# Performance work log

Hardware: AMD Instinct MI355X
Metric: run time of the kernel (lower is better)

The kernel has to match this reference:

```python
import jax, jax.numpy as jnp
import numpy as np
from jax import lax

D = 512      # d_model
DSRC = 128   # grapheme vocab
DTGT = 128   # phoneme vocab
B = 1024
TS = 64      # T_src
TT = 64      # T_tgt


def setup_inputs() -> dict:
    key = jax.random.key(0)
    ks = iter(jax.random.split(key, 64))
    def w(shape, s=0.02):
        return (jax.random.normal(next(ks), shape) * s).astype(jnp.float32)
    z = lambda n: jnp.zeros((n,), jnp.float32)
    inp = dict(
        src=jax.random.randint(next(ks), (B, TS), 0, DSRC),
        tgt=jax.random.randint(next(ks), (B, TT), 0, DTGT),
        enc_emb_w=w((DSRC, D)),
        # PyTorch LSTM gate order i,f,g,o; weights stored [in, 4H] for x @ W
        enc_wi_f=w((D, 4 * D)), enc_wh_f=w((D, 4 * D)), enc_bi_f=z(4 * D), enc_bh_f=z(4 * D),
        enc_wi_b=w((D, 4 * D)), enc_wh_b=w((D, 4 * D)), enc_bi_b=z(4 * D), enc_bh_b=z(4 * D),
        enc_post_w=w((2 * D, D)), enc_post_b=z(D),
        h_post_w=w((2 * D, D)), h_post_b=z(D),
        c_post_w=w((2 * D, D)), c_post_b=z(D),
        wq_w=w((D, D)), wq_b=z(D),
        wk_w=w((D, D)), wk_b=z(D),
        wv_w=w((D, D)), wv_b=z(D),
        wo_w=w((D, D)), wo_b=z(D),
        dec_emb_w=w((DTGT, D)),
        dec_wi=w((2 * D, 4 * D)), dec_wh=w((D, 4 * D)), dec_bi=z(4 * D), dec_bh=z(4 * D),
        dec_post_w=w((D, DTGT)), dec_post_b=z(DTGT),
    )
    return inp


def _lstm_cell(x, h, c, Wi, Wh, b):
    g = x @ Wi + h @ Wh + b
    i, f, gg, o = jnp.split(g, 4, axis=-1)
    c = jax.nn.sigmoid(f) * c + jax.nn.sigmoid(i) * jnp.tanh(gg)
    h = jax.nn.sigmoid(o) * jnp.tanh(c)
    return h, c


def _lstm_scan(x, h0, c0, Wi, Wh, b):
    # x: [B,T,Din] -> ys: [B,T,H], final (h,c)
    def step(carry, xt):
        h, c = _lstm_cell(xt, carry[0], carry[1], Wi, Wh, b)
        return (h, c), h
    (h, c), ys = lax.scan(step, (h0, c0), jnp.swapaxes(x, 0, 1))
    return jnp.swapaxes(ys, 0, 1), h, c


def reference(src, tgt, enc_emb_w,
              enc_wi_f, enc_wh_f, enc_bi_f, enc_bh_f,
              enc_wi_b, enc_wh_b, enc_bi_b, enc_bh_b,
              enc_post_w, enc_post_b, h_post_w, h_post_b, c_post_w, c_post_b,
              wq_w, wq_b, wk_w, wk_b, wv_w, wv_b, wo_w, wo_b,
              dec_emb_w, dec_wi, dec_wh, dec_bi, dec_bh, dec_post_w, dec_post_b):
    b, d = src.shape[0], enc_emb_w.shape[1]
    scale = d ** -0.5
    z0 = jnp.zeros((b, d), enc_emb_w.dtype)

    # --- bi-LSTM encoder (dropout = identity in eval) ---
    emb = enc_emb_w[src]                                   # [B,TS,D]
    fwd, hf, cf = _lstm_scan(emb, z0, z0, enc_wi_f, enc_wh_f, enc_bi_f + enc_bh_f)
    bwd, hb, cb = _lstm_scan(emb[:, ::-1], z0, z0, enc_wi_b, enc_wh_b, enc_bi_b + enc_bh_b)
    bwd = bwd[:, ::-1]
    enc_out = jnp.concatenate([fwd, bwd], -1) @ enc_post_w + enc_post_b   # [B,TS,D]
    h = jnp.tanh(jnp.concatenate([hf, hb], -1) @ h_post_w + h_post_b)     # [B,D]
    c = jnp.tanh(jnp.concatenate([cf, cb], -1) @ c_post_w + c_post_b)

    # attention K/V projections of enc_out are step-invariant: compute once
    K = enc_out @ wk_w + wk_b
    V = enc_out @ wv_w + wv_b
    dec_b = dec_bi + dec_bh

    prev = dec_emb_w[tgt[:, 0]]                            # [B,D]

    def dec_step(carry, _):
        prev, h, c = carry
        q = prev @ wq_w + wq_b                             # [B,D]
        score = jax.nn.softmax(jnp.einsum('bd,btd->bt', q, K) * scale)  # [B,TS]
        ctx = jnp.einsum('bt,btd->bd', score, V) @ wo_w + wo_b
        x = jnp.concatenate([prev, ctx], -1)               # [B,2D]
        h, c = _lstm_cell(x, h, c, dec_wi, dec_wh, dec_b)
        out = h @ dec_post_w + dec_post_b                  # [B,DTGT]
        prev = dec_emb_w[jnp.argmax(out, -1)]
        return (prev, h, c), (score, out)

    _, (attn_res, res) = lax.scan(dec_step, (prev, h, c), None, length=tgt.shape[1])
    attn_res = jnp.swapaxes(attn_res, 0, 1)                # [B,TT,TS]
    res = jnp.swapaxes(res, 0, 1)                          # [B,TT,DTGT]
    return attn_res, res
```

## Files before the change

kernel.cpp:

```cpp
#include <hip/hip_runtime.h>
#include <hip/hip_bf16.h>

namespace k77 {

typedef long long ll;
typedef double f64x4 __attribute__((ext_vector_type(4)));

constexpr int D    = 512;
constexpr int DTGT = 128;
constexpr int NB   = 1024;
constexpr int TS   = 64;
constexpr int TT   = 64;
constexpr int G4   = 2048;

__global__ void probe_mfma(int* __restrict__ dlay)
{
    __shared__ double ref[256];
    __shared__ int ok[4];
    const int l = threadIdx.x;
    const int l15 = l & 15, l4 = l >> 4;
    if (l < 4) ok[l] = 1;
    double a = 1.0 + 3.0 * l15 + 7.0 * l4;
    double b = 2.0 + 5.0 * l15 + 11.0 * l4;
    f64x4 d = {0.0, 0.0, 0.0, 0.0};
    d = __builtin_amdgcn_mfma_f64_16x16x4f64(a, b, d, 0, 0, 0);
    if (l < 16) {
        for (int j = 0; j < 16; ++j) {
            double s = 0.0;
            for (int k = 0; k < 4; ++k)
                s += (1.0 + 3.0 * l + 7.0 * k) * (2.0 + 5.0 * j + 11.0 * k);
            ref[l * 16 + j] = s;
        }
    }
    __syncthreads();
#pragma unroll
    for (int n = 0; n < 4; ++n) {
        if (d[n] != ref[(l4 * 4 + n) * 16 + l15]) atomicAnd(&ok[0], 0);
        if (d[n] != ref[(l4 + 4 * n) * 16 + l15]) atomicAnd(&ok[1], 0);
        if (d[n] != ref[l15 * 16 + (l4 * 4 + n)]) atomicAnd(&ok[2], 0);
        if (d[n] != ref[l15 * 16 + (l4 + 4 * n)]) atomicAnd(&ok[3], 0);
    }
    __syncthreads();
    if (l == 0) {
        int r = -1;
        for (int i = 3; i >= 0; --i) if (ok[i]) r = i;
        *dlay = r;
    }
}

__global__ void dlay_check(const int* __restrict__ dlay, float* __restrict__ out0)
{
    if (*dlay < 0)
        for (int i = threadIdx.x; i < 256; i += 64) out0[i] = 3.0e38f;
}

__device__ __forceinline__ void dmap(int dl, int l15, int l4, int n, int& r, int& c)
{
    if (dl == 1)      { r = l4 + 4 * n;  c = l15; }
    else if (dl == 2) { r = l15;         c = l4 * 4 + n; }
    else if (dl == 3) { r = l15;         c = l4 + 4 * n; }
    else              { r = l4 * 4 + n;  c = l15; }
}

__global__ void tab_gemm64(const float* __restrict__ A, const float* __restrict__ B,
                           const float* __restrict__ b1, const float* __restrict__ b2,
                           float* __restrict__ C, int M, int N, int K, int ldc, float scale, int perm)
{
    int j = blockIdx.x * 256 + threadIdx.x;
    int m = blockIdx.y;
    if (j >= N || m >= M) return;
    const float* ar = A + (size_t)m * K;
    double acc = 0.0;
    for (int k = 0; k < K; ++k) acc += (double)ar[k] * (double)B[(size_t)k * N + j];
    if (b1) acc += (double)b1[j];
    if (b2) acc += (double)b2[j];
    int j2 = perm ? ((j & 511) * 4 + (j >> 9)) : j;
    C[(size_t)m * ldc + j2] = (float)(acc * (double)scale);
}

struct Tab3 { const float *A0,*A1,*A2,*B0,*B1,*B2,*p0,*p1,*p2,*q0,*q1,*q2; float *C0,*C1,*C2; };
__global__ void tab3_gemm64(Tab3 t)
{
    int j = blockIdx.x * 256 + threadIdx.x;
    int m = blockIdx.y;
    int z = blockIdx.z;
    const float* A  = z == 0 ? t.A0 : (z == 1 ? t.A1 : t.A2);
    const float* B  = z == 0 ? t.B0 : (z == 1 ? t.B1 : t.B2);
    const float* b1 = z == 0 ? t.p0 : (z == 1 ? t.p1 : t.p2);
    const float* b2 = z == 0 ? t.q0 : (z == 1 ? t.q1 : t.q2);
    float*       C  = z == 0 ? t.C0 : (z == 1 ? t.C1 : t.C2);
    const float* ar = A + (size_t)m * D;
    double acc = 0.0;
    for (int k = 0; k < D; ++k) acc += (double)ar[k] * (double)B[(size_t)k * G4 + j];
    acc += (double)b1[j];
    acc += (double)b2[j];
    C[(size_t)m * G4 + (j & 511) * 4 + (j >> 9)] = (float)acc;
}

struct Perm4 { const float *i0,*i1,*i2,*i3; float *o0,*o1,*o2,*o3; int r0,r1,r2,r3; };
__global__ void permW4(Perm4 p)
{
    int j = blockIdx.x * 256 + threadIdx.x;
    int k = blockIdx.y;
    int z = blockIdx.z;
    const float* in = z == 0 ? p.i0 : (z == 1 ? p.i1 : (z == 2 ? p.i2 : p.i3));
    float*      out = z == 0 ? p.o0 : (z == 1 ? p.o1 : (z == 2 ? p.o2 : p.o3));
    int      rowoff = z == 0 ? p.r0 : (z == 1 ? p.r1 : (z == 2 ? p.r2 : p.r3));
    out[(size_t)k * G4 + (j & 511) * 4 + (j >> 9)] = in[(size_t)(k + rowoff) * G4 + j];
}

__global__ void init_kv(const float* __restrict__ bkvo, __hip_bfloat16* __restrict__ Kb,
                        float* __restrict__ Vb)
{
    for (ll i = (ll)blockIdx.x * 256 + threadIdx.x; i < (ll)NB * TS * D; i += (ll)gridDim.x * 256) {
        int d = (int)(i & (D - 1));
        Kb[i] = __float2bfloat16(bkvo[d]);
        Vb[i] = bkvo[D + d];
    }
}

template<int USE2>
__device__ __forceinline__ void gates_body(
    double* smem, const float* a0, const float* a1,
    const float* B0, const float* B1,
    const float* tab, const int* idx, int idxStride,
    float* cb, float* hb, int bx, int by, int K, int useC, int dl, int tid)
{
    float* As = (float*)smem;
    float* Bs = As + 64 * 34;
    const int row0 = by * 64, col0 = bx * 32;
    const int wave = tid >> 6, lane = tid & 63;
    const int wr = wave >> 1, wc = wave & 1;
    const int l15 = lane & 15, l4 = lane >> 4;

    f64x4 acc[2];
    acc[0] = (f64x4){0.0, 0.0, 0.0, 0.0};
    acc[1] = (f64x4){0.0, 0.0, 0.0, 0.0};

    for (int k0 = 0; k0 < K; k0 += 32) {
#pragma unroll
        for (int l = 0; l < 8; ++l) {
            int t = tid + l * 256;
            int k = t & 31, m = t >> 5;
            int kk = k0 + k;
            float v;
            if (USE2 && kk >= D) v = a1[(size_t)(row0 + m) * D + (kk - D)];
            else                 v = a0[(size_t)(row0 + m) * D + kk];
            As[m * 34 + k] = v;
        }
#pragma unroll
        for (int l = 0; l < 4; ++l) {
            int t = tid + l * 256;
            int j = t & 31, kr = t >> 5;
            int kk = k0 + kr;
            float v;
            if (USE2 && kk >= D) v = B1[(size_t)(kk - D) * G4 + col0 + j];
            else                 v = B0[(size_t)kk * G4 + col0 + j];
            Bs[j * 35 + kr] = v;
        }
        __syncthreads();
#pragma unroll
        for (int kk4 = 0; kk4 < 8; ++kk4) {
            const int kr = kk4 * 4 + l4;
            double a0f = (double)As[(wr * 32 + l15) * 34 + kr];
            double a1f = (double)As[(wr * 32 + 16 + l15) * 34 + kr];
            double b0f = (double)Bs[(wc * 16 + l15) * 35 + kr];
            acc[0] = __builtin_amdgcn_mfma_f64_16x16x4f64(a0f, b0f, acc[0], 0, 0, 0);
            acc[1] = __builtin_amdgcn_mfma_f64_16x16x4f64(a1f, b0f, acc[1], 0, 0, 0);
        }
        __syncthreads();
    }

    float* G = (float*)smem;
#pragma unroll
    for (int tr = 0; tr < 2; ++tr)
#pragma unroll
        for (int n = 0; n < 4; ++n) {
            int r, c;
            dmap(dl, l15, l4, n, r, c);
            int lr = wr * 32 + tr * 16 + r;
            int lc = wc * 16 + c;
            const float* trw = tab + (size_t)idx[(size_t)(row0 + lr) * idxStride] * G4;
            G[lr * 33 + lc] = (float)(acc[tr][n] + (double)trw[col0 + lc]);
        }
    __syncthreads();

    const int ty = tid >> 3, tx = tid & 7;
    const int d  = (col0 + tx * 4) >> 2;
#pragma unroll
    for (int i = 0; i < 2; ++i) {
        int rl  = ty * 2 + i;
        int row = row0 + rl;
        float gi = G[rl * 33 + tx * 4 + 0];
        float gf = G[rl * 33 + tx * 4 + 1];
        float gg = G[rl * 33 + tx * 4 + 2];
        float go = G[rl * 33 + tx * 4 + 3];
        float c  = useC ? cb[(size_t)row * D + d] : 0.f;
        float si = 1.f / (1.f + expf(-gi));
        float sf = 1.f / (1.f + expf(-gf));
        float so = 1.f / (1.f + expf(-go));
        c = sf * c + si * tanhf(gg);
        cb[(size_t)row * D + d] = c;
        hb[(size_t)row * D + d] = so * tanhf(c);
    }
}

__device__ __forceinline__ void fold_body(
    double* smem, const float* h, const float* W, int rowoff,
    __hip_bfloat16* Kb, float* Vb, int trow, int bx, int by, int dl, int tid)
{
    float* As = (float*)smem;
    float* Bs = As + 64 * 34;
    const int row0 = by * 64, col0 = bx * 64;
    const int wave = tid >> 6, lane = tid & 63;
    const int wr = wave >> 1, wc = wave & 1;
    const int l15 = lane & 15, l4 = lane >> 4;

    f64x4 acc[2][2];
#pragma unroll
    for (int i = 0; i < 2; ++i)
#pragma unroll
        for (int j = 0; j < 2; ++j) acc[i][j] = (f64x4){0.0, 0.0, 0.0, 0.0};

    for (int k0 = 0; k0 < D; k0 += 32) {
#pragma unroll
        for (int l = 0; l < 8; ++l) {
            int t = tid + l * 256;
            {   int k = t & 31, m = t >> 5;
                As[m * 34 + k] = h[(size_t)(row0 + m) * D + k0 + k];
            }
            {   int j = t & 63, kr = t >> 6;
                Bs[j * 35 + kr] = W[(size_t)(rowoff + k0 + kr) * 1024 + col0 + j];
            }
        }
        __syncthreads();
#pragma unroll
        for (int kk4 = 0; kk4 < 8; ++kk4) {
            const int kr = kk4 * 4 + l4;
            double a0f = (double)As[(wr * 32 + l15) * 34 + kr];
            double a1f = (double)As[(wr * 32 + 16 + l15) * 34 + kr];
            double b0f = (double)Bs[(wc * 32 + l15) * 35 + kr];
            double b1f = (double)Bs[(wc * 32 + 16 + l15) * 35 + kr];
            acc[0][0] = __builtin_amdgcn_mfma_f64_16x16x4f64(a0f, b0f, acc[0][0], 0, 0, 0);
            acc[0][1] = __builtin_amdgcn_mfma_f64_16x16x4f64(a0f, b1f, acc[0][1], 0, 0, 0);
            acc[1][0] = __builtin_amdgcn_mfma_f64_16x16x4f64(a1f, b0f, acc[1][0], 0, 0, 0);
            acc[1][1] = __builtin_amdgcn_mfma_f64_16x16x4f64(a1f, b1f, acc[1][1], 0, 0, 0);
        }
        __syncthreads();
    }

#pragma unroll
    for (int tr = 0; tr < 2; ++tr)
#pragma unroll
        for (int tc = 0; tc < 2; ++tc)
#pragma unroll
            for (int n = 0; n < 4; ++n) {
                int r, c;
                dmap(dl, l15, l4, n, r, c);
                int row = row0 + wr * 32 + tr * 16 + r;
                int col = col0 + wc * 32 + tc * 16 + c;
                double v = acc[tr][tc][n];
                ll ix = ((ll)row * TS + trow) * D + (col & (D - 1));
                if (col < D) {
                    double v2 = v + (double)__bfloat162float(Kb[ix]);
                    Kb[ix] = __float2bfloat16((float)v2);
                } else {
                    Vb[ix] = (float)((double)Vb[ix] + v);
                }
            }
}

struct EncArgs {
    const float *hFr, *hBr;
    float *hFw, *hBw, *cF, *cB;
    const float *WhPf, *WhPb, *tabPf, *tabPb;
    const int *srcF, *srcB;
    const float *WKVo;
    __hip_bfloat16 *Kb; float *Vb;
    int foldF, foldB;
    int K, useC, nG;
    const int *dlayp;
};

__global__ __launch_bounds__(256)
void enc_mega(EncArgs a)
{
    __shared__ double smem[2208];
    const int bid = blockIdx.x;
    const int tid = threadIdx.x;
    const int dl  = a.dlayp[0];
    if (bid < a.nG) {
        const int dir = bid >> 10;
        const int tt  = bid & 1023;
        gates_body<0>(smem,
                      dir ? a.hBr : a.hFr, nullptr,
                      dir ? a.WhPb : a.WhPf, nullptr,
                      dir ? a.tabPb : a.tabPf,
                      dir ? a.srcB : a.srcF, TS,
                      dir ? a.cB : a.cF,
                      dir ? a.hBw : a.hFw,
                      tt & 63, tt >> 6, a.K, a.useC, dl, tid);
    } else {
        const int ff = bid - a.nG;
        const int fz = ff >> 8;
        fold_body(smem, fz ? a.hBr : a.hFr, a.WKVo, fz ? D : 0,
                  a.Kb, a.Vb, fz ? a.foldB : a.foldF,
                  ff & 15, (ff >> 4) & 15, dl, tid);
    }
}

struct DGArgs {
    const float *ctx, *h;
    const float *wiP, *whP, *tabP;
    const int *amax;
    float *cdec, *hw;
    const int *dlayp;
};

__global__ __launch_bounds__(256)
void dec_gates(DGArgs a)
{
    __shared__ double smem[1648];
    const int bid = blockIdx.x;
    gates_body<1>(smem, a.ctx, a.h, a.wiP, a.whP, a.tabP,
                  a.amax, 1, a.cdec, a.hw, bid & 63, bid >> 6, 2 * D, 1,
                  a.dlayp[0], threadIdx.x);
}

__global__ void attn_kernel(const float* __restrict__ qtab, const int* __restrict__ amax,
                            const __hip_bfloat16* __restrict__ Kb, const float* __restrict__ Vb,
                            float* __restrict__ aout, int step, float* __restrict__ ctx)
{
    const int b = blockIdx.x, tid = threadIdx.x;
    __shared__ float qs[D];
    __shared__ float ss[TS];
    qs[tid] = qtab[(size_t)amax[b] * D + tid];
    __syncthreads();
    const int t = tid >> 3, l8 = tid & 7;
    const __hip_bfloat16* krow = Kb + ((size_t)b * TS + t) * D;
    double acc = 0.0;
    for (int d = l8; d < D; d += 8) acc += (double)qs[d] * (double)__bfloat162float(krow[d]);
    acc += __shfl_xor(acc, 4);
    acc += __shfl_xor(acc, 2);
    acc += __shfl_xor(acc, 1);
    if (l8 == 0) ss[t] = (float)acc;
    __syncthreads();
    if (tid < TS) {
        float v = ss[tid], mx = v;
#pragma unroll
        for (int o = 32; o; o >>= 1) mx = fmaxf(mx, __shfl_xor(mx, o));
        float e = expf(v - mx), sm = e;
#pragma unroll
        for (int o = 32; o; o >>= 1) sm += __shfl_xor(sm, o);
        float sc = e / sm;
        ss[tid] = sc;
        aout[((size_t)b * TT + step) * TS + tid] = sc;
    }
    __syncthreads();
    double a = 0.0;
    const float* vcol = Vb + (size_t)b * TS * D + tid;
    for (int t2 = 0; t2 < TS; ++t2) a += (double)ss[t2] * (double)vcol[(size_t)t2 * D];
    ctx[(size_t)b * D + tid] = (float)a;
}

__global__ __launch_bounds__(512)
void out_attn(const float* __restrict__ h, const float* __restrict__ W,
              const float* __restrict__ bias, float* __restrict__ res,
              int step, int* __restrict__ amax,
              const float* __restrict__ qtab, const __hip_bfloat16* __restrict__ Kb,
              const float* __restrict__ Vb, float* __restrict__ aout,
              float* __restrict__ ctx, int doAttn)
{
    const int b = blockIdx.x, tid = threadIdx.x;
    __shared__ float hs[D];
    __shared__ double vals[DTGT];
    __shared__ int tok;
    __shared__ float qs[D];
    __shared__ float ss[TS];

    hs[tid] = h[(size_t)b * D + tid];
    __syncthreads();
    if (tid < DTGT) {
        double acc = (double)bias[tid];
        for (int k = 0; k < D; ++k) acc += (double)hs[k] * (double)W[(size_t)k * DTGT + tid];
        vals[tid] = acc;
        res[((size_t)b * TT + step) * DTGT + tid] = (float)acc;
    }
    __syncthreads();
    if (tid == 0) {
        double best = vals[0]; int bi = 0;
        for (int j = 1; j < DTGT; ++j) if (vals[j] > best) { best = vals[j]; bi = j; }
        amax[b] = bi;
        tok = bi;
    }
    __syncthreads();

    if (!doAttn) return;

    qs[tid] = qtab[(size_t)tok * D + tid];
    __syncthreads();
    const int t = tid >> 3, l8 = tid & 7;
    const __hip_bfloat16* krow = Kb + ((size_t)b * TS + t) * D;
    double acc = 0.0;
    for (int d = l8; d < D; d += 8) acc += (double)qs[d] * (double)__bfloat162float(krow[d]);
    acc += __shfl_xor(acc, 4);
    acc += __shfl_xor(acc, 2);
    acc += __shfl_xor(acc, 1);
    if (l8 == 0) ss[t] = (float)acc;
    __syncthreads();
    if (tid < TS) {
        float v = ss[tid], mx = v;
#pragma unroll
        for (int o = 32; o; o >>= 1) mx = fmaxf(mx, __shfl_xor(mx, o));
        float e = expf(v - mx), sm = e;
#pragma unroll
        for (int o = 32; o; o >>= 1) sm += __shfl_xor(sm, o);
        float sc = e / sm;
        ss[tid] = sc;
        aout[((size_t)b * TT + (step + 1)) * TS + tid] = sc;
    }
    __syncthreads();
    double a = 0.0;
    const float* vcol = Vb + (size_t)b * TS * D + tid;
    for (int t2 = 0; t2 < TS; ++t2) a += (double)ss[t2] * (double)vcol[(size_t)t2 * D];
    ctx[(size_t)b * D + tid] = (float)a;
}

__global__ __launch_bounds__(512)
void hc_init(const float* __restrict__ hF, const float* __restrict__ hB,
             const float* __restrict__ cF, const float* __restrict__ cB,
             const float* __restrict__ hpw, const float* __restrict__ hpb,
             const float* __restrict__ cpw, const float* __restrict__ cpb,
             float* __restrict__ h0, float* __restrict__ c0)
{
    __shared__ float s0[D], s1[D], s2[D], s3[D];
    const int b = blockIdx.x, j = threadIdx.x;
    s0[j] = hF[(size_t)b * D + j]; s1[j] = hB[(size_t)b * D + j];
    s2[j] = cF[(size_t)b * D + j]; s3[j] = cB[(size_t)b * D + j];
    __syncthreads();
    double a = (double)hpb[j];
    for (int k = 0; k < D; ++k) a += (double)s0[k] * (double)hpw[(size_t)k * D + j];
    for (int k = 0; k < D; ++k) a += (double)s1[k] * (double)hpw[(size_t)(k + D) * D + j];
    h0[(size_t)b * D + j] = (float)tanh(a);
    a = (double)cpb[j];
    for (int k = 0; k < D; ++k) a += (double)s2[k] * (double)cpw[(size_t)k * D + j];
    for (int k = 0; k < D; ++k) a += (double)s3[k] * (double)cpw[(size_t)(k + D) * D + j];
    c0[(size_t)b * D + j] = (float)tanh(a);
}

__global__ void init_amax(const int* __restrict__ tgt, int* __restrict__ amax)
{
    int b = blockIdx.x * 256 + threadIdx.x;
    if (b < NB) amax[b] = tgt[(size_t)b * TT];
}

}

extern "C" void kernel_launch(void* const* d_in, const int* in_sizes, int n_in,
                              void* d_out, int out_size, void* d_ws, size_t ws_size,
                              hipStream_t stream)
{
    using namespace k77;
    (void)in_sizes; (void)n_in; (void)out_size;

    const int*   src        = (const int*)  d_in[0];
    const int*   tgt        = (const int*)  d_in[1];
    const float* enc_emb_w  = (const float*)d_in[2];
    const float* enc_wi_f   = (const float*)d_in[3];
    const float* enc_wh_f   = (const float*)d_in[4];
    const float* enc_bi_f   = (const float*)d_in[5];
    const float* enc_bh_f   = (const float*)d_in[6];
    const float* enc_wi_b   = (const float*)d_in[7];
    const float* enc_wh_b   = (const float*)d_in[8];
    const float* enc_bi_b   = (const float*)d_in[9];
    const float* enc_bh_b   = (const float*)d_in[10];
    const float* enc_post_w = (const float*)d_in[11];
    const float* enc_post_b = (const float*)d_in[12];
    const float* h_post_w   = (const float*)d_in[13];
    const float* h_post_b   = (const float*)d_in[14];
    const float* c_post_w   = (const float*)d_in[15];
    const float* c_post_b   = (const float*)d_in[16];
    const float* wq_w       = (const float*)d_in[17];
    const float* wq_b       = (const float*)d_in[18];
    const float* wk_w       = (const float*)d_in[19];
    const float* wk_b       = (const float*)d_in[20];
    const float* wv_w       = (const float*)d_in[21];
    const float* wv_b       = (const float*)d_in[22];
    const float* wo_w       = (const float*)d_in[23];
    const float* wo_b       = (const float*)d_in[24];
    const float* dec_emb_w  = (const float*)d_in[25];
    const float* dec_wi     = (const float*)d_in[26];
    const float* dec_wh     = (const float*)d_in[27];
    const float* dec_bi     = (const float*)d_in[28];
    const float* dec_bh     = (const float*)d_in[29];
    const float* dec_post_w = (const float*)d_in[30];
    const float* dec_post_b = (const float*)d_in[31];

    float* ws = (float*)d_ws;
    size_t off = 0;
    auto alloc = [&](size_t n) { float* p = ws + off; off += n; return p; };
    float* hF0     = alloc((size_t)NB * D);
    float* hF1     = alloc((size_t)NB * D);
    float* hB0     = alloc((size_t)NB * D);
    float* hB1     = alloc((size_t)NB * D);
    float* cF      = alloc((size_t)NB * D);
    float* cB      = alloc((size_t)NB * D);
    float* hd0     = alloc((size_t)NB * D);
    float* hd1     = alloc((size_t)NB * D);
    float* cdec    = alloc((size_t)NB * D);
    float* ctxb    = alloc((size_t)NB * D);
    float* tabPf   = alloc((size_t)128 * G4);
    float* tabPb   = alloc((size_t)128 * G4);
    float* dec_tabP= alloc((size_t)128 * G4);
    float* q_tab   = alloc((size_t)128 * D);
    float* WKVo    = alloc((size_t)1024 * 1024);
    float* bkvo    = alloc(1024);
    float* WhPf    = alloc((size_t)D * G4);
    float* WhPb    = alloc((size_t)D * G4);
    float* dec_wiP = alloc((size_t)D * G4);
    float* dec_whP = alloc((size_t)D * G4);
    float* Wv_tmp  = alloc((size_t)1024 * D);
    float* bv_tmp  = alloc(D);
    int*   amax    = (int*)alloc(1024);
    int*   dlayD   = (int*)alloc(64);

    const size_t commonF = off;
    const size_t kvCnt   = (size_t)NB * TS * D;
    const size_t need    = commonF * 4 + kvCnt * 2 + kvCnt * 4;

    if (ws_size < need) {
        hipMemsetAsync(d_out, 0x7F, 1024, stream);
        return;
    }
    __hip_bfloat16* Kh = (__hip_bfloat16*)(ws + commonF);
    float*          Vf = (float*)((char*)Kh + kvCnt * 2);

    float* attn_out = (float*)d_out;
    float* res_out  = attn_out + (size_t)NB * TT * TS;

    const float scale = 0.044194173824159216f;

    float* hFbuf[2] = {hF0, hF1};
    float* hBbuf[2] = {hB0, hB1};
    float* hd[2]    = {hd0, hd1};

    probe_mfma<<<1, 64, 0, stream>>>(dlayD);
    dlay_check<<<1, 64, 0, stream>>>(dlayD, attn_out);

    Tab3 t3;
    t3.A0 = enc_emb_w; t3.A1 = enc_emb_w; t3.A2 = dec_emb_w;
    t3.B0 = enc_wi_f;  t3.B1 = enc_wi_b;  t3.B2 = dec_wi;
    t3.p0 = enc_bi_f;  t3.p1 = enc_bi_b;  t3.p2 = dec_bi;
    t3.q0 = enc_bh_f;  t3.q1 = enc_bh_b;  t3.q2 = dec_bh;
    t3.C0 = tabPf;     t3.C1 = tabPb;     t3.C2 = dec_tabP;
    tab3_gemm64<<<dim3(8, 128, 3), 256, 0, stream>>>(t3);
    tab_gemm64<<<dim3(2, 128), 256, 0, stream>>>(dec_emb_w, wq_w, wq_b, nullptr, q_tab, 128, D, D, D, scale, 0);
    tab_gemm64<<<dim3(2, 1024), 256, 0, stream>>>(enc_post_w, wk_w, nullptr, nullptr, WKVo, 1024, D, D, 1024, 1.f, 0);
    tab_gemm64<<<dim3(2, 1024), 256, 0, stream>>>(enc_post_w, wv_w, nullptr, nullptr, Wv_tmp, 1024, D, D, D, 1.f, 0);
    tab_gemm64<<<dim3(2, 1024), 256, 0, stream>>>(Wv_tmp, wo_w, nullptr, nullptr, WKVo + D, 1024, D, D, 1024, 1.f, 0);
    tab_gemm64<<<dim3(2, 1), 256, 0, stream>>>(enc_post_b, wk_w, wk_b, nullptr, bkvo, 1, D, D, D, 1.f, 0);
    tab_gemm64<<<dim3(2, 1), 256, 0, stream>>>(enc_post_b, wv_w, wv_b, nullptr, bv_tmp, 1, D, D, D, 1.f, 0);
    tab_gemm64<<<dim3(2, 1), 256, 0, stream>>>(bv_tmp, wo_w, wo_b, nullptr, bkvo + D, 1, D, D, D, 1.f, 0);
    Perm4 p4;
    p4.i0 = enc_wh_f; p4.o0 = WhPf;    p4.r0 = 0;
    p4.i1 = enc_wh_b; p4.o1 = WhPb;    p4.r1 = 0;
    p4.i2 = dec_wi;   p4.o2 = dec_wiP; p4.r2 = 512;
    p4.i3 = dec_wh;   p4.o3 = dec_whP; p4.r3 = 0;
    permW4<<<dim3(8, 512, 4), 256, 0, stream>>>(p4);
    init_kv<<<2048, 256, 0, stream>>>(bkvo, Kh, Vf);

    for (int t = 0; t < TS; ++t) {
        EncArgs ea;
        ea.hFr = hFbuf[t & 1]; ea.hBr = hBbuf[t & 1];
        ea.hFw = hFbuf[(t + 1) & 1]; ea.hBw = hBbuf[(t + 1) & 1];
        ea.cF = cF; ea.cB = cB;
        ea.WhPf = WhPf; ea.WhPb = WhPb; ea.tabPf = tabPf; ea.tabPb = tabPb;
        ea.srcF = src + t; ea.srcB = src + (TS - 1 - t);
        ea.WKVo = WKVo; ea.Kb = Kh; ea.Vb = Vf;
        ea.foldF = t - 1; ea.foldB = TS - t;
        ea.K = t ? D : 0; ea.useC = t ? 1 : 0; ea.nG = 2048;
        ea.dlayp = dlayD;
        const int grid = 2048 + (t ? 512 : 0);
        enc_mega<<<grid, 256, 0, stream>>>(ea);
    }
    {
        EncArgs ea;
        ea.hFr = hFbuf[0]; ea.hBr = hBbuf[0];
        ea.hFw = nullptr; ea.hBw = nullptr; ea.cF = cF; ea.cB = cB;
        ea.WhPf = WhPf; ea.WhPb = WhPb; ea.tabPf = tabPf; ea.tabPb = tabPb;
        ea.srcF = src; ea.srcB = src;
        ea.WKVo = WKVo; ea.Kb = Kh; ea.Vb = Vf;
        ea.foldF = 63; ea.foldB = 0;
        ea.K = 0; ea.useC = 0; ea.nG = 0;
        ea.dlayp = dlayD;
        enc_mega<<<512, 256, 0, stream>>>(ea);
    }

    hc_init<<<NB, 512, 0, stream>>>(hFbuf[0], hBbuf[0], cF, cB,
                                    h_post_w, h_post_b, c_post_w, c_post_b, hd0, cdec);
    init_amax<<<4, 256, 0, stream>>>(tgt, amax);

    attn_kernel<<<NB, 512, 0, stream>>>(q_tab, amax, Kh, Vf, attn_out, 0, ctxb);
    for (int st = 0; st < TT; ++st) {
        DGArgs da;
        da.ctx = ctxb; da.h = hd[st & 1];
        da.wiP = dec_wiP; da.whP = dec_whP; da.tabP = dec_tabP;
        da.amax = amax; da.cdec = cdec; da.hw = hd[(st + 1) & 1];
        da.dlayp = dlayD;
        dec_gates<<<1024, 256, 0, stream>>>(da);
        out_attn<<<NB, 512, 0, stream>>>(hd[(st + 1) & 1], dec_post_w, dec_post_b, res_out,
                                         st, amax, q_tab, Kh, Vf, attn_out, ctxb,
                                         st < TT - 1 ? 1 : 0);
    }
}
```

Baseline: 20.65 ms.

## Register-prefetch next K-tile in gate and fold GEMMs; split output projection across threads

The gate and fold FP64-MFMA GEMM loops now load the next 32-wide K slice of A and B into registers while the current slice is being multiplied from shared memory. This hides global-load latency behind compute at the cost of more registers. The out_attn kernel also spreads the 512x128 output projection over all 512 threads as four partial sums of 128 k-values each, instead of using only 128 threads. This shortens the serial dot-product chain per thread. The extra summation order changes double-precision rounding only slightly.

```diff
diff --git a/kernel.cpp b/kernel.cpp
--- a/kernel.cpp
+++ b/kernel.cpp
@@ -137,28 +137,49 @@
     acc[0] = (f64x4){0.0, 0.0, 0.0, 0.0};
     acc[1] = (f64x4){0.0, 0.0, 0.0, 0.0};
 
+    float ra[8], rb[4];
+    if (K > 0) {
+#pragma unroll
+        for (int l = 0; l < 8; ++l) {
+            int t = tid + l * 256; int k = t & 31, m = t >> 5;
+            if (USE2 && k >= D) ra[l] = a1[(size_t)(row0 + m) * D + (k - D)];
+            else                ra[l] = a0[(size_t)(row0 + m) * D + k];
+        }
+#pragma unroll
+        for (int l = 0; l < 4; ++l) {
+            int t = tid + l * 256; int j = t & 31, kr = t >> 5;
+            if (USE2 && kr >= D) rb[l] = B1[(size_t)(kr - D) * G4 + col0 + j];
+            else                 rb[l] = B0[(size_t)kr * G4 + col0 + j];
+        }
+    }
+
     for (int k0 = 0; k0 < K; k0 += 32) {
 #pragma unroll
         for (int l = 0; l < 8; ++l) {
             int t = tid + l * 256;
-            int k = t & 31, m = t >> 5;
-            int kk = k0 + k;
-            float v;
-            if (USE2 && kk >= D) v = a1[(size_t)(row0 + m) * D + (kk - D)];
-            else                 v = a0[(size_t)(row0 + m) * D + kk];
-            As[m * 34 + k] = v;
+            As[(t >> 5) * 34 + (t & 31)] = ra[l];
         }
 #pragma unroll
         for (int l = 0; l < 4; ++l) {
             int t = tid + l * 256;
-            int j = t & 31, kr = t >> 5;
-            int kk = k0 + kr;
-            float v;
-            if (USE2 && kk >= D) v = B1[(size_t)(kk - D) * G4 + col0 + j];
-            else                 v = B0[(size_t)kk * G4 + col0 + j];
-            Bs[j * 35 + kr] = v;
+            Bs[(t & 31) * 35 + (t >> 5)] = rb[l];
         }
         __syncthreads();
+        if (k0 + 32 < K) {
+            const int kn = k0 + 32;
+#pragma unroll
+            for (int l = 0; l < 8; ++l) {
+                int t = tid + l * 256; int k = kn + (t & 31), m = t >> 5;
+                if (USE2 && k >= D) ra[l] = a1[(size_t)(row0 + m) * D + (k - D)];
+                else                ra[l] = a0[(size_t)(row0 + m) * D + k];
+            }
+#pragma unroll
+            for (int l = 0; l < 4; ++l) {
+                int t = tid + l * 256; int j = t & 31, kr = kn + (t >> 5);
+                if (USE2 && kr >= D) rb[l] = B1[(size_t)(kr - D) * G4 + col0 + j];
+                else                 rb[l] = B0[(size_t)kr * G4 + col0 + j];
+            }
+        }
 #pragma unroll
         for (int kk4 = 0; kk4 < 8; ++kk4) {
             const int kr = kk4 * 4 + l4;
@@ -222,18 +243,31 @@
 #pragma unroll
         for (int j = 0; j < 2; ++j) acc[i][j] = (f64x4){0.0, 0.0, 0.0, 0.0};
 
+    float ra[8], rb[8];
+#pragma unroll
+    for (int l = 0; l < 8; ++l) {
+        int t = tid + l * 256;
+        { int k = t & 31, m = t >> 5; ra[l] = h[(size_t)(row0 + m) * D + k]; }
+        { int j = t & 63, kr = t >> 6; rb[l] = W[(size_t)(rowoff + kr) * 1024 + col0 + j]; }
+    }
+
     for (int k0 = 0; k0 < D; k0 += 32) {
 #pragma unroll
         for (int l = 0; l < 8; ++l) {
             int t = tid + l * 256;
-            {   int k = t & 31, m = t >> 5;
-                As[m * 34 + k] = h[(size_t)(row0 + m) * D + k0 + k];
+            As[(t >> 5) * 34 + (t & 31)] = ra[l];
+            Bs[(t & 63) * 35 + (t >> 6)] = rb[l];
+        }
+        __syncthreads();
+        if (k0 + 32 < D) {
+            const int kn = k0 + 32;
+#pragma unroll
+            for (int l = 0; l < 8; ++l) {
+                int t = tid + l * 256;
+                { int k = kn + (t & 31), m = t >> 5; ra[l] = h[(size_t)(row0 + m) * D + k]; }
+                { int j = t & 63, kr = kn + (t >> 6); rb[l] = W[(size_t)(rowoff + kr) * 1024 + col0 + j]; }
             }
-            {   int j = t & 63, kr = t >> 6;
-                Bs[j * 35 + kr] = W[(size_t)(rowoff + k0 + kr) * 1024 + col0 + j];
-            }
-        }
-        __syncthreads();
+        }
 #pragma unroll
         for (int kk4 = 0; kk4 < 8; ++kk4) {
             const int kr = kk4 * 4 + l4;
@@ -373,23 +407,31 @@
 {
     const int b = blockIdx.x, tid = threadIdx.x;
     __shared__ float hs[D];
-    __shared__ double vals[DTGT];
+    __shared__ double part[4][DTGT];
     __shared__ int tok;
     __shared__ float qs[D];
     __shared__ float ss[TS];
 
     hs[tid] = h[(size_t)b * D + tid];
     __syncthreads();
+    {
+        const int col = tid & 127, pp = tid >> 7;
+        double acc = 0.0;
+        const int kb = pp * 128;
+        for (int k = kb; k < kb + 128; ++k)
+            acc += (double)hs[k] * (double)W[(size_t)k * DTGT + col];
+        part[pp][col] = acc;
+    }
+    __syncthreads();
     if (tid < DTGT) {
-        double acc = (double)bias[tid];
-        for (int k = 0; k < D; ++k) acc += (double)hs[k] * (double)W[(size_t)k * DTGT + tid];
-        vals[tid] = acc;
+        double acc = (double)bias[tid] + part[0][tid] + part[1][tid] + part[2][tid] + part[3][tid];
+        part[0][tid] = acc;
         res[((size_t)b * TT + step) * DTGT + tid] = (float)acc;
     }
     __syncthreads();
     if (tid == 0) {
-        double best = vals[0]; int bi = 0;
-        for (int j = 1; j < DTGT; ++j) if (vals[j] > best) { best = vals[j]; bi = j; }
+        double best = part[0][0]; int bi = 0;
+        for (int j = 1; j < DTGT; ++j) if (part[0][j] > best) { best = part[0][j]; bi = j; }
         amax[b] = bi;
         tok = bi;
     }
```

New measurement: 20.99 ms. About the same (+1.6%).
